# Kernel tuning notes

Measured on AMD Instinct MI355X. Metric: run time of the kernel, lower is better.

## Reference

```python
import jax, jax.numpy as jnp
import numpy as np


def setup_inputs() -> dict:
    key = jax.random.key(0)
    ks = jax.random.split(key, 16)
    B, T, H, E, V = 64, 512, 512, 512, 50257
    sc = 0.02  # weight init scale
    return {
        "enc_seq": jax.random.normal(ks[0], (B, T, H), jnp.float32),
        "enc_mask": jax.random.randint(ks[1], (B, T), 0, 2).astype(jnp.int32),
        "h0": jax.random.normal(ks[2], (1, B, H), jnp.float32),
        "c0": jax.random.normal(ks[3], (1, B, H), jnp.float32),
        "bos_id": 1,
        "eos_id": 2,
        "max_len": 28,
        "emb": jax.random.normal(ks[4], (V, E), jnp.float32) * sc,
        "W_h": jax.random.normal(ks[5], (H, H), jnp.float32) * sc,
        "W_s": jax.random.normal(ks[6], (H, H), jnp.float32) * sc,
        "v": jax.random.normal(ks[7], (H,), jnp.float32) * sc,
        "W_ih": jax.random.normal(ks[8], (4 * H, E + H), jnp.float32) * sc,
        "W_hh": jax.random.normal(ks[9], (4 * H, H), jnp.float32) * sc,
        "b_ih": jnp.zeros((4 * H,), jnp.float32),
        "b_hh": jnp.zeros((4 * H,), jnp.float32),
        "W_out": jax.random.normal(ks[10], (V, H), jnp.float32) * sc,
        "b_out": jnp.zeros((V,), jnp.float32),
    }


def reference(enc_seq, enc_mask, h0, c0, bos_id, eos_id, max_len,
              emb, W_h, W_s, v, W_ih, W_hh, b_ih, b_hh, W_out, b_out):
    B = enc_seq.shape[0]
    h = h0[0]  # [B, H]  (torch: transpose(0,1).squeeze(1))
    c = c0[0]
    # W_h(enc_seq) is loop-invariant; precompute once (same math as per-step recompute)
    Wh_enc = jnp.einsum('bth,kh->btk', enc_seq, W_h)  # [B, T, H]
    neg_inf = jnp.float32(-1e9)
    y0 = jnp.full((B,), bos_id, dtype=jnp.int32)

    def step(carry, _):
        h, c, y = carry
        e_t = emb[y]                                            # [B, E]
        s = h @ W_s.T                                           # [B, H]
        scores = jnp.einsum('bth,h->bt', jnp.tanh(Wh_enc + s[:, None, :]), v)
        scores = jnp.where(enc_mask == 0, neg_inf, scores)
        a = jax.nn.softmax(scores, axis=1)                      # [B, T]
        ctx = jnp.einsum('bt,bth->bh', a, enc_seq)              # [B, H]
        x = jnp.concatenate([e_t, ctx], axis=-1)                # [B, E+H]
        gates = x @ W_ih.T + h @ W_hh.T + b_ih + b_hh           # [B, 4H]
        i, f, g, o = jnp.split(gates, 4, axis=-1)               # torch gate order i,f,g,o
        c2 = jax.nn.sigmoid(f) * c + jax.nn.sigmoid(i) * jnp.tanh(g)
        h2 = jax.nn.sigmoid(o) * jnp.tanh(c2)
        # dropout is identity in eval mode (greedy decoding)
        logits = h2 @ W_out.T + b_out                           # [B, V]
        y2 = jnp.argmax(logits, axis=-1).astype(jnp.int32)
        return (h2, c2, y2), y2

    _, ys = jax.lax.scan(step, (h, c, y0), None, length=max_len - 1)
    return ys.T  # [B, max_len-1] greedy token ids
```

## Files before the change

kernel.cpp:

```cpp
#include <hip/hip_runtime.h>
#include <hip/hip_bf16.h>
#include <cmath>


#define TKK 16

__global__ __launch_bounds__(256) void gemm_tile(
    const float* __restrict__ A, int lda,
    const float* __restrict__ B, int ldb,
    float* __restrict__ C, int ldc,
    int Kchunk, long long c_zstride)
{
  __shared__ __align__(16) float At[TKK][68];
  __shared__ __align__(16) float Bt[TKK][132];
  const int tid = threadIdx.x;
  const int tx = tid & 15, ty = tid >> 4;
  const long long mbase = (long long)blockIdx.y * 64;
  const long long nbase = (long long)blockIdx.x * 128;
  const int kbase = blockIdx.z * Kchunk;
  const float* Ap = A + mbase * lda + kbase;
  const float* Bp = B + nbase * ldb + kbase;
  float acc[4][8];
#pragma unroll
  for (int i = 0; i < 4; i++)
#pragma unroll
    for (int j = 0; j < 8; j++) acc[i][j] = 0.f;

  const int lm = tid >> 2;
  const int lk = (tid & 3) << 2;
  for (int k0 = 0; k0 < Kchunk; k0 += TKK) {
    float4 av = *(const float4*)(Ap + (long long)lm * lda + k0 + lk);
    At[lk + 0][lm] = av.x; At[lk + 1][lm] = av.y;
    At[lk + 2][lm] = av.z; At[lk + 3][lm] = av.w;
#pragma unroll
    for (int r = 0; r < 2; r++) {
      int n = (tid + r * 256) >> 2;
      float4 bv = *(const float4*)(Bp + (long long)n * ldb + k0 + lk);
      Bt[lk + 0][n] = bv.x; Bt[lk + 1][n] = bv.y;
      Bt[lk + 2][n] = bv.z; Bt[lk + 3][n] = bv.w;
    }
    __syncthreads();
#pragma unroll
    for (int kk = 0; kk < TKK; ++kk) {
      float4 a4 = *(const float4*)&At[kk][ty * 4];
      float4 b0 = *(const float4*)&Bt[kk][tx * 8];
      float4 b1 = *(const float4*)&Bt[kk][tx * 8 + 4];
      float as[4] = {a4.x, a4.y, a4.z, a4.w};
      float bs[8] = {b0.x, b0.y, b0.z, b0.w, b1.x, b1.y, b1.z, b1.w};
#pragma unroll
      for (int i = 0; i < 4; i++)
#pragma unroll
        for (int j = 0; j < 8; j++)
          acc[i][j] = fmaf(as[i], bs[j], acc[i][j]);
    }
    __syncthreads();
  }
  float* Cp = C + (long long)blockIdx.z * c_zstride;
#pragma unroll
  for (int i = 0; i < 4; i++) {
    long long m = mbase + ty * 4 + i;
#pragma unroll
    for (int j = 0; j < 8; j += 4) {
      float4 v;
      v.x = acc[i][j]; v.y = acc[i][j + 1]; v.z = acc[i][j + 2]; v.w = acc[i][j + 3];
      *(float4*)(Cp + m * ldc + nbase + tx * 8 + j) = v;
    }
  }
}

__global__ __launch_bounds__(256) void wcat_kernel(
    const float* __restrict__ W_ih, const float* __restrict__ W_hh,
    float* __restrict__ wcat)
{
  long long fi = (long long)blockIdx.x * 256 + threadIdx.x;
  if (fi >= 2048LL * 1536 / 4) return;
  int k = (int)(fi / 384);
  int c = (int)(fi % 384) * 4;
  float4 v;
  if (c < 1024) v = *(const float4*)(W_ih + (long long)k * 1024 + c);
  else          v = *(const float4*)(W_hh + (long long)k * 512 + (c - 1024));
  *(float4*)(wcat + fi * 4) = v;
}

__global__ __launch_bounds__(256) void init_kernel(
    const float* __restrict__ h0, const float* __restrict__ c0,
    const int* __restrict__ bos,
    float* __restrict__ h, float* __restrict__ c, int* __restrict__ y)
{
  int i = blockIdx.x * 256 + threadIdx.x;
  if (i < 64 * 512) { h[i] = h0[i]; c[i] = c0[i]; }
  if (i < 64) y[i] = bos[0];
}

__global__ __launch_bounds__(256) void scores_kernel(
    const float* __restrict__ whenc,
    const float* __restrict__ spart,
    const float* __restrict__ vvec,
    const int* __restrict__ mask,
    float* __restrict__ scores)
{
  const int b = blockIdx.x, tc = blockIdx.y, tid = threadIdx.x;
  __shared__ __align__(16) float sS[512];
  __shared__ __align__(16) float sV[512];
  for (int i = tid; i < 512; i += 256) {
    sS[i] = spart[0 * 64 * 512 + b * 512 + i] + spart[1 * 64 * 512 + b * 512 + i]
          + spart[2 * 64 * 512 + b * 512 + i] + spart[3 * 64 * 512 + b * 512 + i];
    sV[i] = vvec[i];
  }
  __syncthreads();
  const int wave = tid >> 6, lane = tid & 63;
  const int t0 = tc * 128 + wave * 32;
  for (int tt = 0; tt < 32; ++tt) {
    int t = t0 + tt;
    const float* row = whenc + ((long long)b * 512 + t) * 512;
    float p = 0.f;
#pragma unroll
    for (int u = 0; u < 2; ++u) {
      int hb = u * 256 + lane * 4;
      float4 w = *(const float4*)(row + hb);
      float4 s4 = *(const float4*)&sS[hb];
      float4 v4 = *(const float4*)&sV[hb];
      p = fmaf(v4.x, tanhf(w.x + s4.x), p);
      p = fmaf(v4.y, tanhf(w.y + s4.y), p);
      p = fmaf(v4.z, tanhf(w.z + s4.z), p);
      p = fmaf(v4.w, tanhf(w.w + s4.w), p);
    }
#pragma unroll
    for (int off = 32; off; off >>= 1) p += __shfl_xor(p, off);
    if (lane == 0)
      scores[b * 512 + t] = mask[b * 512 + t] ? p : -1e9f;
  }
}

__global__ __launch_bounds__(256) void ctx_kernel(
    const float* __restrict__ scores,
    const float* __restrict__ enc,
    float* __restrict__ ctxp)
{
  const int b = blockIdx.x, tc = blockIdx.y, tid = threadIdx.x;
  __shared__ float sc[512];
  __shared__ float red[256];
  float l0 = scores[b * 512 + tid];
  float l1 = scores[b * 512 + 256 + tid];
  red[tid] = fmaxf(l0, l1);
  __syncthreads();
  for (int s = 128; s > 0; s >>= 1) {
    if (tid < s) red[tid] = fmaxf(red[tid], red[tid + s]);
    __syncthreads();
  }
  float mx = red[0];
  __syncthreads();
  float e0 = expf(l0 - mx), e1 = expf(l1 - mx);
  sc[tid] = e0; sc[tid + 256] = e1;
  red[tid] = e0 + e1;
  __syncthreads();
  for (int s = 128; s > 0; s >>= 1) {
    if (tid < s) red[tid] += red[tid + s];
    __syncthreads();
  }
  float inv = 1.f / red[0];
  float a0 = 0.f, a1 = 0.f;
  for (int u = 0; u < 128; ++u) {
    int t = tc * 128 + u;
    float w = sc[t] * inv;
    const float* row = enc + ((long long)b * 512 + t) * 512;
    float2 e = *(const float2*)(row + tid * 2);
    a0 = fmaf(w, e.x, a0);
    a1 = fmaf(w, e.y, a1);
  }
  float2 o; o.x = a0; o.y = a1;
  *(float2*)(ctxp + ((long long)(b * 4 + tc)) * 512 + tid * 2) = o;
}

__global__ __launch_bounds__(256) void xbuild_kernel(
    const float* __restrict__ emb, const int* __restrict__ y,
    const float* __restrict__ ctxp, const float* __restrict__ h,
    float* __restrict__ x)
{
  const int b = blockIdx.x, tid = threadIdx.x;
  const int yb = y[b];
  for (int i = tid; i < 1536; i += 256) {
    float val;
    if (i < 512) {
      val = emb[(long long)yb * 512 + i];
    } else if (i < 1024) {
      int hh = i - 512;
      val = ctxp[(b * 4 + 0) * 512 + hh] + ctxp[(b * 4 + 1) * 512 + hh]
          + ctxp[(b * 4 + 2) * 512 + hh] + ctxp[(b * 4 + 3) * 512 + hh];
    } else {
      val = h[b * 512 + (i - 1024)];
    }
    x[b * 1536 + i] = val;
  }
}

__global__ __launch_bounds__(512) void lstm_kernel(
    const float* __restrict__ gpart,
    const float* __restrict__ b_ih, const float* __restrict__ b_hh,
    float* __restrict__ h, float* __restrict__ c)
{
  const int b = blockIdx.x, hc = threadIdx.x;
  float g[4];
#pragma unroll
  for (int q = 0; q < 4; q++) {
    int k = q * 512 + hc;
    float s = b_ih[k] + b_hh[k];
    s += gpart[(0 * 64 + b) * 2048 + k];
    s += gpart[(1 * 64 + b) * 2048 + k];
    s += gpart[(2 * 64 + b) * 2048 + k];
    g[q] = s;
  }
  float ig = 1.f / (1.f + expf(-g[0]));
  float fg = 1.f / (1.f + expf(-g[1]));
  float gg = tanhf(g[2]);
  float og = 1.f / (1.f + expf(-g[3]));
  float c2 = fg * c[b * 512 + hc] + ig * gg;
  float h2 = og * tanhf(c2);
  c[b * 512 + hc] = c2;
  h[b * 512 + hc] = h2;
}

__global__ __launch_bounds__(256) void logits_kernel(
    const float* __restrict__ A,
    const float* __restrict__ W,
    const float* __restrict__ bias,
    int V, float* __restrict__ pval, int* __restrict__ pidx, int nvc)
{
  __shared__ __align__(16) float At[TKK][68];
  __shared__ __align__(16) float Bt[TKK][132];
  __shared__ float lv[64][16];
  __shared__ int   li[64][16];
  const int tid = threadIdx.x;
  const int tx = tid & 15, ty = tid >> 4;
  const int nbase = blockIdx.x * 128;
  float acc[4][8];
#pragma unroll
  for (int i = 0; i < 4; i++)
#pragma unroll
    for (int j = 0; j < 8; j++) acc[i][j] = 0.f;
  const int lm = tid >> 2;
  const int lk = (tid & 3) << 2;
  for (int k0 = 0; k0 < 512; k0 += TKK) {
    float4 av = *(const float4*)(A + lm * 512 + k0 + lk);
    At[lk + 0][lm] = av.x; At[lk + 1][lm] = av.y;
    At[lk + 2][lm] = av.z; At[lk + 3][lm] = av.w;
#pragma unroll
    for (int r = 0; r < 2; r++) {
      int n = (tid + r * 256) >> 2;
      int ng = nbase + n;
      float4 bv = make_float4(0.f, 0.f, 0.f, 0.f);
      if (ng < V) bv = *(const float4*)(W + (long long)ng * 512 + k0 + lk);
      Bt[lk + 0][n] = bv.x; Bt[lk + 1][n] = bv.y;
      Bt[lk + 2][n] = bv.z; Bt[lk + 3][n] = bv.w;
    }
    __syncthreads();
#pragma unroll
    for (int kk = 0; kk < TKK; ++kk) {
      float4 a4 = *(const float4*)&At[kk][ty * 4];
      float4 b0 = *(const float4*)&Bt[kk][tx * 8];
      float4 b1 = *(const float4*)&Bt[kk][tx * 8 + 4];
      float as[4] = {a4.x, a4.y, a4.z, a4.w};
      float bs[8] = {b0.x, b0.y, b0.z, b0.w, b1.x, b1.y, b1.z, b1.w};
#pragma unroll
      for (int i = 0; i < 4; i++)
#pragma unroll
        for (int j = 0; j < 8; j++)
          acc[i][j] = fmaf(as[i], bs[j], acc[i][j]);
    }
    __syncthreads();
  }
#pragma unroll
  for (int i = 0; i < 4; i++) {
    float bv_ = -INFINITY; int bi_ = 0x7fffffff;
#pragma unroll
    for (int j = 0; j < 8; j++) {
      int vg = nbase + tx * 8 + j;
      if (vg < V) {
        float val = acc[i][j] + bias[vg];
        if (val > bv_) { bv_ = val; bi_ = vg; }
      }
    }
    lv[ty * 4 + i][tx] = bv_; li[ty * 4 + i][tx] = bi_;
  }
  __syncthreads();
  if (tid < 64) {
    float bv_ = -INFINITY; int bi_ = 0x7fffffff;
#pragma unroll
    for (int t = 0; t < 16; t++) {
      if (lv[tid][t] > bv_) { bv_ = lv[tid][t]; bi_ = li[tid][t]; }
    }
    pval[tid * nvc + blockIdx.x] = bv_;
    pidx[tid * nvc + blockIdx.x] = bi_;
  }
}

__global__ __launch_bounds__(64) void argfinal_kernel(
    const float* __restrict__ pval, const int* __restrict__ pidx, int nvc,
    int* __restrict__ y, int* __restrict__ out, int step, int steps)
{
  const int b = blockIdx.x, lane = threadIdx.x;
  float bv = -INFINITY; int bi = 0x7fffffff;
  for (int ci = lane; ci < nvc; ci += 64) {
    float v = pval[b * nvc + ci];
    int ix = pidx[b * nvc + ci];
    if (v > bv || (v == bv && ix < bi)) { bv = v; bi = ix; }
  }
#pragma unroll
  for (int off = 32; off; off >>= 1) {
    float ov = __shfl_xor(bv, off);
    int oi = __shfl_xor(bi, off);
    if (ov > bv || (ov == bv && oi < bi)) { bv = ov; bi = oi; }
  }
  if (lane == 0) { y[b] = bi; out[b * steps + step] = bi; }
}

extern "C" void kernel_launch(void* const* d_in, const int* in_sizes, int n_in,
                              void* d_out, int out_size, void* d_ws, size_t ws_size,
                              hipStream_t stream) {
  const float* enc_seq = (const float*)d_in[0];
  const int*   enc_mask = (const int*)d_in[1];
  const float* h0 = (const float*)d_in[2];
  const float* c0 = (const float*)d_in[3];
  const int*   bos = (const int*)d_in[4];
  const float* emb = (const float*)d_in[7];
  const float* W_h = (const float*)d_in[8];
  const float* W_s = (const float*)d_in[9];
  const float* vvec = (const float*)d_in[10];
  const float* W_ih = (const float*)d_in[11];
  const float* W_hh = (const float*)d_in[12];
  const float* b_ih = (const float*)d_in[13];
  const float* b_hh = (const float*)d_in[14];
  const float* W_out = (const float*)d_in[15];
  const float* b_out = (const float*)d_in[16];

  const int B = 64, T = 512, H = 512;
  const int V = in_sizes[16];
  const int steps = out_size / B;
  const int NVC = (V + 127) / 128;
  int* out = (int*)d_out;

  float* ws = (float*)d_ws;
  size_t off = 0;
  auto alloc = [&](size_t n) { float* p = ws + off; off += (n + 15) & ~(size_t)15; return p; };
  float* whenc  = alloc((size_t)B * T * H);
  float* scores = alloc((size_t)B * T);
  float* spart  = alloc(4ull * B * H);
  float* ctxp   = alloc((size_t)B * 4 * H);
  float* xbuf   = alloc((size_t)B * 1536);
  float* gpart  = alloc(3ull * B * 2048);
  float* wcat   = alloc(2048ull * 1536);
  float* hbuf   = alloc((size_t)B * H);
  float* cbuf   = alloc((size_t)B * H);
  float* pval   = alloc((size_t)B * NVC);
  int*   ybuf   = (int*)alloc(B);
  int*   pidx   = (int*)alloc((size_t)B * NVC);
  (void)ws_size;

  init_kernel<<<128, 256, 0, stream>>>(h0, c0, bos, hbuf, cbuf, ybuf);
  wcat_kernel<<<3072, 256, 0, stream>>>(W_ih, W_hh, wcat);

  gemm_tile<<<dim3(4, 512, 1), 256, 0, stream>>>(
      enc_seq, 512, W_h, 512, whenc, 512, 512, 0);

  for (int step = 0; step < steps; ++step) {
    gemm_tile<<<dim3(4, 1, 4), 256, 0, stream>>>(
        hbuf, 512, W_s, 512, spart, 512, 128, (long long)B * H);
    scores_kernel<<<dim3(64, 4), 256, 0, stream>>>(whenc, spart, vvec, enc_mask, scores);
    ctx_kernel<<<dim3(64, 4), 256, 0, stream>>>(scores, enc_seq, ctxp);
    xbuild_kernel<<<64, 256, 0, stream>>>(emb, ybuf, ctxp, hbuf, xbuf);
    gemm_tile<<<dim3(16, 1, 3), 256, 0, stream>>>(
        xbuf, 1536, wcat, 1536, gpart, 2048, 512, (long long)B * 2048);
    lstm_kernel<<<64, 512, 0, stream>>>(gpart, b_ih, b_hh, hbuf, cbuf);
    logits_kernel<<<NVC, 256, 0, stream>>>(hbuf, W_out, b_out, V, pval, pidx, NVC);
    argfinal_kernel<<<64, 64, 0, stream>>>(pval, pidx, NVC, ybuf, out, step, steps);
  }
}
```

Before: 6.069 ms.

## Use split-bf16 MFMA for per-step GEMMs and logits with fused argmax

```diff
diff --git a/kernel.cpp b/kernel.cpp
--- a/kernel.cpp
+++ b/kernel.cpp
@@ -4,6 +4,20 @@
 
 
 #define TKK 16
+
+typedef __attribute__((ext_vector_type(8))) short bf16x8;
+typedef __attribute__((ext_vector_type(4))) float f32x4;
+
+__device__ inline unsigned short bf16rn(float x) {
+  unsigned int u = __float_as_uint(x);
+  unsigned int r = u + 0x7fffu + ((u >> 16) & 1u);
+  return (unsigned short)(r >> 16);
+}
+__device__ inline void split1(float x, unsigned short& h, unsigned short& l) {
+  h = bf16rn(x);
+  float hf = __uint_as_float(((unsigned int)h) << 16);
+  l = bf16rn(x - hf);
+}
 
 __global__ __launch_bounds__(256) void gemm_tile(
     const float* __restrict__ A, int lda,
@@ -43,8 +57,8 @@
 #pragma unroll
     for (int kk = 0; kk < TKK; ++kk) {
       float4 a4 = *(const float4*)&At[kk][ty * 4];
-      float4 b0 = *(const float4*)&Bt[kk][tx * 8];
-      float4 b1 = *(const float4*)&Bt[kk][tx * 8 + 4];
+      float4 b0 = *(const float4*)&Bt[kk][tx * 4];
+      float4 b1 = *(const float4*)&Bt[kk][64 + tx * 4];
       float as[4] = {a4.x, a4.y, a4.z, a4.w};
       float bs[8] = {b0.x, b0.y, b0.z, b0.w, b1.x, b1.y, b1.z, b1.w};
 #pragma unroll
@@ -59,12 +73,11 @@
 #pragma unroll
   for (int i = 0; i < 4; i++) {
     long long m = mbase + ty * 4 + i;
-#pragma unroll
-    for (int j = 0; j < 8; j += 4) {
-      float4 v;
-      v.x = acc[i][j]; v.y = acc[i][j + 1]; v.z = acc[i][j + 2]; v.w = acc[i][j + 3];
-      *(float4*)(Cp + m * ldc + nbase + tx * 8 + j) = v;
-    }
+    float4 v0, v1;
+    v0.x = acc[i][0]; v0.y = acc[i][1]; v0.z = acc[i][2]; v0.w = acc[i][3];
+    v1.x = acc[i][4]; v1.y = acc[i][5]; v1.z = acc[i][6]; v1.w = acc[i][7];
+    *(float4*)(Cp + m * ldc + nbase + tx * 4) = v0;
+    *(float4*)(Cp + m * ldc + nbase + 64 + tx * 4) = v1;
   }
 }
 
@@ -82,19 +95,62 @@
   *(float4*)(wcat + fi * 4) = v;
 }
 
+__global__ __launch_bounds__(256) void wcat_split_kernel(
+    const float* __restrict__ W_ih, const float* __restrict__ W_hh,
+    unsigned short* __restrict__ whi, unsigned short* __restrict__ wlo)
+{
+  long long fi = (long long)blockIdx.x * 256 + threadIdx.x;
+  if (fi >= 2048LL * 1536 / 4) return;
+  int k = (int)(fi / 384);
+  int c = (int)(fi % 384) * 4;
+  float4 v;
+  if (c < 1024) v = *(const float4*)(W_ih + (long long)k * 1024 + c);
+  else          v = *(const float4*)(W_hh + (long long)k * 512 + (c - 1024));
+  long long e = fi * 4;
+  float xs[4] = {v.x, v.y, v.z, v.w};
+#pragma unroll
+  for (int q = 0; q < 4; q++) {
+    unsigned short h, l; split1(xs[q], h, l);
+    whi[e + q] = h; wlo[e + q] = l;
+  }
+}
+
+__global__ __launch_bounds__(256) void split_kernel(
+    const float* __restrict__ src, unsigned short* __restrict__ hi,
+    unsigned short* __restrict__ lo, long long n)
+{
+  long long i = (long long)blockIdx.x * 256 + threadIdx.x;
+  long long stride = (long long)gridDim.x * 256;
+  for (long long e = i * 4; e < n; e += stride * 4) {
+    float4 v = *(const float4*)(src + e);
+    float xs[4] = {v.x, v.y, v.z, v.w};
+#pragma unroll
+    for (int q = 0; q < 4; q++) {
+      unsigned short h, l; split1(xs[q], h, l);
+      hi[e + q] = h; lo[e + q] = l;
+    }
+  }
+}
+
 __global__ __launch_bounds__(256) void init_kernel(
     const float* __restrict__ h0, const float* __restrict__ c0,
     const int* __restrict__ bos,
-    float* __restrict__ h, float* __restrict__ c, int* __restrict__ y)
+    float* __restrict__ h, float* __restrict__ c, int* __restrict__ y,
+    unsigned short* __restrict__ h_hi, unsigned short* __restrict__ h_lo)
 {
   int i = blockIdx.x * 256 + threadIdx.x;
-  if (i < 64 * 512) { h[i] = h0[i]; c[i] = c0[i]; }
+  if (i < 64 * 512) {
+    float hv = h0[i];
+    h[i] = hv; c[i] = c0[i];
+    unsigned short hh, hl; split1(hv, hh, hl);
+    h_hi[i] = hh; h_lo[i] = hl;
+  }
   if (i < 64) y[i] = bos[0];
 }
 
 __global__ __launch_bounds__(256) void scores_kernel(
     const float* __restrict__ whenc,
-    const float* __restrict__ spart,
+    const float* __restrict__ spart, int np,
     const float* __restrict__ vvec,
     const int* __restrict__ mask,
     float* __restrict__ scores)
@@ -103,8 +159,9 @@
   __shared__ __align__(16) float sS[512];
   __shared__ __align__(16) float sV[512];
   for (int i = tid; i < 512; i += 256) {
-    sS[i] = spart[0 * 64 * 512 + b * 512 + i] + spart[1 * 64 * 512 + b * 512 + i]
-          + spart[2 * 64 * 512 + b * 512 + i] + spart[3 * 64 * 512 + b * 512 + i];
+    float s = 0.f;
+    for (int p = 0; p < np; ++p) s += spart[(long long)p * 64 * 512 + b * 512 + i];
+    sS[i] = s;
     sV[i] = vvec[i];
   }
   __syncthreads();
@@ -175,7 +232,8 @@
 __global__ __launch_bounds__(256) void xbuild_kernel(
     const float* __restrict__ emb, const int* __restrict__ y,
     const float* __restrict__ ctxp, const float* __restrict__ h,
-    float* __restrict__ x)
+    float* __restrict__ xf,
+    unsigned short* __restrict__ xhi, unsigned short* __restrict__ xlo)
 {
   const int b = blockIdx.x, tid = threadIdx.x;
   const int yb = y[b];
@@ -190,14 +248,19 @@
     } else {
       val = h[b * 512 + (i - 1024)];
     }
-    x[b * 1536 + i] = val;
+    if (xf) xf[b * 1536 + i] = val;
+    if (xhi) {
+      unsigned short hh2, ll2; split1(val, hh2, ll2);
+      xhi[b * 1536 + i] = hh2; xlo[b * 1536 + i] = ll2;
+    }
   }
 }
 
 __global__ __launch_bounds__(512) void lstm_kernel(
-    const float* __restrict__ gpart,
+    const float* __restrict__ gpart, int ngparts,
     const float* __restrict__ b_ih, const float* __restrict__ b_hh,
-    float* __restrict__ h, float* __restrict__ c)
+    float* __restrict__ h, float* __restrict__ c,
+    unsigned short* __restrict__ h_hi, unsigned short* __restrict__ h_lo)
 {
   const int b = blockIdx.x, hc = threadIdx.x;
   float g[4];
@@ -205,9 +268,8 @@
   for (int q = 0; q < 4; q++) {
     int k = q * 512 + hc;
     float s = b_ih[k] + b_hh[k];
-    s += gpart[(0 * 64 + b) * 2048 + k];
-    s += gpart[(1 * 64 + b) * 2048 + k];
-    s += gpart[(2 * 64 + b) * 2048 + k];
+    for (int p = 0; p < ngparts; ++p)
+      s += gpart[((long long)p * 64 + b) * 2048 + k];
     g[q] = s;
   }
   float ig = 1.f / (1.f + expf(-g[0]));
@@ -218,6 +280,105 @@
   float h2 = og * tanhf(c2);
   c[b * 512 + hc] = c2;
   h[b * 512 + hc] = h2;
+  if (h_hi) {
+    unsigned short hh, hl; split1(h2, hh, hl);
+    h_hi[b * 512 + hc] = hh; h_lo[b * 512 + hc] = hl;
+  }
+}
+
+__global__ __launch_bounds__(256) void mfma_gemm(
+    const unsigned short* __restrict__ Ahi, const unsigned short* __restrict__ Alo,
+    const unsigned short* __restrict__ Bhi, const unsigned short* __restrict__ Blo,
+    float* __restrict__ C, int K, int N)
+{
+  const int tid = threadIdx.x;
+  const int w = tid >> 6, l = tid & 63;
+  const int arow = blockIdx.y * 64 + w * 16 + (l & 15);
+  const int koff = (l >> 4) * 8;
+  const int nbase = blockIdx.x * 64;
+  f32x4 acc[4];
+#pragma unroll
+  for (int cf = 0; cf < 4; ++cf) acc[cf] = (f32x4){0.f, 0.f, 0.f, 0.f};
+
+  for (int k0 = 0; k0 < K; k0 += 32) {
+    bf16x8 ahi = *(const bf16x8*)(Ahi + (size_t)arow * K + k0 + koff);
+    bf16x8 alo = *(const bf16x8*)(Alo + (size_t)arow * K + k0 + koff);
+#pragma unroll
+    for (int cf = 0; cf < 4; ++cf) {
+      int col = nbase + cf * 16 + (l & 15);
+      bf16x8 bhi = *(const bf16x8*)(Bhi + (size_t)col * K + k0 + koff);
+      bf16x8 blo = *(const bf16x8*)(Blo + (size_t)col * K + k0 + koff);
+      acc[cf] = __builtin_amdgcn_mfma_f32_16x16x32_bf16(ahi, bhi, acc[cf], 0, 0, 0);
+      acc[cf] = __builtin_amdgcn_mfma_f32_16x16x32_bf16(ahi, blo, acc[cf], 0, 0, 0);
+      acc[cf] = __builtin_amdgcn_mfma_f32_16x16x32_bf16(alo, bhi, acc[cf], 0, 0, 0);
+    }
+  }
+#pragma unroll
+  for (int cf = 0; cf < 4; ++cf) {
+    int col = nbase + cf * 16 + (l & 15);
+#pragma unroll
+    for (int j = 0; j < 4; ++j) {
+      int rowc = blockIdx.y * 64 + w * 16 + (l >> 4) * 4 + j;
+      C[(size_t)rowc * N + col] = acc[cf][j];
+    }
+  }
+}
+
+__global__ __launch_bounds__(256) void mfma_logits(
+    const unsigned short* __restrict__ Ahi, const unsigned short* __restrict__ Alo,
+    const unsigned short* __restrict__ Bhi, const unsigned short* __restrict__ Blo,
+    const float* __restrict__ bias, int V, int K,
+    float* __restrict__ pval, int* __restrict__ pidx, int nvc)
+{
+  const int tid = threadIdx.x;
+  const int w = tid >> 6, l = tid & 63;
+  const int arow = w * 16 + (l & 15);
+  const int koff = (l >> 4) * 8;
+  const int nbase = blockIdx.x * 64;
+  const bf16x8 bz = {0, 0, 0, 0, 0, 0, 0, 0};
+  f32x4 acc[4];
+#pragma unroll
+  for (int cf = 0; cf < 4; ++cf) acc[cf] = (f32x4){0.f, 0.f, 0.f, 0.f};
+
+  for (int k0 = 0; k0 < K; k0 += 32) {
+    bf16x8 ahi = *(const bf16x8*)(Ahi + (size_t)arow * K + k0 + koff);
+    bf16x8 alo = *(const bf16x8*)(Alo + (size_t)arow * K + k0 + koff);
+#pragma unroll
+    for (int cf = 0; cf < 4; ++cf) {
+      int col = nbase + cf * 16 + (l & 15);
+      bf16x8 bhi = bz, blo = bz;
+      if (col < V) {
+        bhi = *(const bf16x8*)(Bhi + (size_t)col * K + k0 + koff);
+        blo = *(const bf16x8*)(Blo + (size_t)col * K + k0 + koff);
+      }
+      acc[cf] = __builtin_amdgcn_mfma_f32_16x16x32_bf16(ahi, bhi, acc[cf], 0, 0, 0);
+      acc[cf] = __builtin_amdgcn_mfma_f32_16x16x32_bf16(ahi, blo, acc[cf], 0, 0, 0);
+      acc[cf] = __builtin_amdgcn_mfma_f32_16x16x32_bf16(alo, bhi, acc[cf], 0, 0, 0);
+    }
+  }
+#pragma unroll
+  for (int j = 0; j < 4; ++j) {
+    float bv = -INFINITY; int bi = 0x7fffffff;
+#pragma unroll
+    for (int cf = 0; cf < 4; ++cf) {
+      int col = nbase + cf * 16 + (l & 15);
+      if (col < V) {
+        float v = acc[cf][j] + bias[col];
+        if (v > bv) { bv = v; bi = col; }
+      }
+    }
+#pragma unroll
+    for (int off = 1; off <= 8; off <<= 1) {
+      float ov = __shfl_xor(bv, off);
+      int oi = __shfl_xor(bi, off);
+      if (ov > bv || (ov == bv && oi < bi)) { bv = ov; bi = oi; }
+    }
+    if ((l & 15) == 0) {
+      int b = w * 16 + (l >> 4) * 4 + j;
+      pval[b * nvc + blockIdx.x] = bv;
+      pidx[b * nvc + blockIdx.x] = bi;
+    }
+  }
 }
 
 __global__ __launch_bounds__(256) void logits_kernel(
@@ -257,8 +418,8 @@
 #pragma unroll
     for (int kk = 0; kk < TKK; ++kk) {
       float4 a4 = *(const float4*)&At[kk][ty * 4];
-      float4 b0 = *(const float4*)&Bt[kk][tx * 8];
-      float4 b1 = *(const float4*)&Bt[kk][tx * 8 + 4];
+      float4 b0 = *(const float4*)&Bt[kk][tx * 4];
+      float4 b1 = *(const float4*)&Bt[kk][64 + tx * 4];
       float as[4] = {a4.x, a4.y, a4.z, a4.w};
       float bs[8] = {b0.x, b0.y, b0.z, b0.w, b1.x, b1.y, b1.z, b1.w};
 #pragma unroll
@@ -274,10 +435,10 @@
     float bv_ = -INFINITY; int bi_ = 0x7fffffff;
 #pragma unroll
     for (int j = 0; j < 8; j++) {
-      int vg = nbase + tx * 8 + j;
+      int vg = (j < 4) ? (nbase + tx * 4 + j) : (nbase + 64 + tx * 4 + (j - 4));
       if (vg < V) {
         float val = acc[i][j] + bias[vg];
-        if (val > bv_) { bv_ = val; bi_ = vg; }
+        if (val > bv_ || (val == bv_ && vg < bi_)) { bv_ = val; bi_ = vg; }
       }
     }
     lv[ty * 4 + i][tx] = bv_; li[ty * 4 + i][tx] = bi_;
@@ -287,7 +448,9 @@
     float bv_ = -INFINITY; int bi_ = 0x7fffffff;
 #pragma unroll
     for (int t = 0; t < 16; t++) {
-      if (lv[tid][t] > bv_) { bv_ = lv[tid][t]; bi_ = li[tid][t]; }
+      if (lv[tid][t] > bv_ || (lv[tid][t] == bv_ && li[tid][t] < bi_)) {
+        bv_ = lv[tid][t]; bi_ = li[tid][t];
+      }
     }
     pval[tid * nvc + blockIdx.x] = bv_;
     pidx[tid * nvc + blockIdx.x] = bi_;
@@ -334,44 +497,101 @@
   const float* b_out = (const float*)d_in[16];
 
   const int B = 64, T = 512, H = 512;
-  const int V = in_sizes[16];
+  const int Vn = in_sizes[15] / 512;
   const int steps = out_size / B;
-  const int NVC = (V + 127) / 128;
   int* out = (int*)d_out;
 
   float* ws = (float*)d_ws;
   size_t off = 0;
   auto alloc = [&](size_t n) { float* p = ws + off; off += (n + 15) & ~(size_t)15; return p; };
-  float* whenc  = alloc((size_t)B * T * H);
-  float* scores = alloc((size_t)B * T);
-  float* spart  = alloc(4ull * B * H);
-  float* ctxp   = alloc((size_t)B * 4 * H);
-  float* xbuf   = alloc((size_t)B * 1536);
-  float* gpart  = alloc(3ull * B * 2048);
-  float* wcat   = alloc(2048ull * 1536);
-  float* hbuf   = alloc((size_t)B * H);
-  float* cbuf   = alloc((size_t)B * H);
-  float* pval   = alloc((size_t)B * NVC);
-  int*   ybuf   = (int*)alloc(B);
-  int*   pidx   = (int*)alloc((size_t)B * NVC);
-  (void)ws_size;
-
-  init_kernel<<<128, 256, 0, stream>>>(h0, c0, bos, hbuf, cbuf, ybuf);
-  wcat_kernel<<<3072, 256, 0, stream>>>(W_ih, W_hh, wcat);
-
-  gemm_tile<<<dim3(4, 512, 1), 256, 0, stream>>>(
-      enc_seq, 512, W_h, 512, whenc, 512, 512, 0);
-
-  for (int step = 0; step < steps; ++step) {
-    gemm_tile<<<dim3(4, 1, 4), 256, 0, stream>>>(
-        hbuf, 512, W_s, 512, spart, 512, 128, (long long)B * H);
-    scores_kernel<<<dim3(64, 4), 256, 0, stream>>>(whenc, spart, vvec, enc_mask, scores);
-    ctx_kernel<<<dim3(64, 4), 256, 0, stream>>>(scores, enc_seq, ctxp);
-    xbuild_kernel<<<64, 256, 0, stream>>>(emb, ybuf, ctxp, hbuf, xbuf);
-    gemm_tile<<<dim3(16, 1, 3), 256, 0, stream>>>(
-        xbuf, 1536, wcat, 1536, gpart, 2048, 512, (long long)B * 2048);
-    lstm_kernel<<<64, 512, 0, stream>>>(gpart, b_ih, b_hh, hbuf, cbuf);
-    logits_kernel<<<NVC, 256, 0, stream>>>(hbuf, W_out, b_out, V, pval, pidx, NVC);
-    argfinal_kernel<<<64, 64, 0, stream>>>(pval, pidx, NVC, ybuf, out, step, steps);
-  }
-}
+
+  const size_t NEW_NEED = 200ull << 20;
+  if (ws_size >= NEW_NEED) {
+    const int NVC = (Vn + 63) / 64;
+    float* whenc  = alloc((size_t)B * T * H);
+    float* sbuf   = alloc((size_t)B * T);
+    float* spartf = alloc((size_t)B * H);
+    float* ctxp   = alloc((size_t)B * 4 * H);
+    float* gbuf   = alloc((size_t)B * 2048);
+    float* hbuf   = alloc((size_t)B * H);
+    float* cbuf   = alloc((size_t)B * H);
+    float* pval   = alloc((size_t)B * NVC);
+    int*   pidx   = (int*)alloc((size_t)B * NVC);
+    int*   ybuf   = (int*)alloc(B);
+    unsigned short* h_hi  = (unsigned short*)alloc((size_t)B * H / 2);
+    unsigned short* h_lo  = (unsigned short*)alloc((size_t)B * H / 2);
+    unsigned short* x_hi  = (unsigned short*)alloc((size_t)B * 1536 / 2);
+    unsigned short* x_lo  = (unsigned short*)alloc((size_t)B * 1536 / 2);
+    unsigned short* ws_hi = (unsigned short*)alloc(512ull * 512 / 2);
+    unsigned short* ws_lo = (unsigned short*)alloc(512ull * 512 / 2);
+    unsigned short* wc_hi = (unsigned short*)alloc(2048ull * 1536 / 2);
+    unsigned short* wc_lo = (unsigned short*)alloc(2048ull * 1536 / 2);
+    unsigned short* wo_hi = (unsigned short*)alloc((size_t)Vn * 512 / 2);
+    unsigned short* wo_lo = (unsigned short*)alloc((size_t)Vn * 512 / 2);
+
+    init_kernel<<<128, 256, 0, stream>>>(h0, c0, bos, hbuf, cbuf, ybuf, h_hi, h_lo);
+    wcat_split_kernel<<<3072, 256, 0, stream>>>(W_ih, W_hh, wc_hi, wc_lo);
+    split_kernel<<<256, 256, 0, stream>>>(W_s, ws_hi, ws_lo, 512ll * 512);
+    split_kernel<<<4096, 256, 0, stream>>>(W_out, wo_hi, wo_lo, (long long)Vn * 512);
+
+    gemm_tile<<<dim3(4, 512, 1), 256, 0, stream>>>(
+        enc_seq, 512, W_h, 512, whenc, 512, 512, 0);
+
+    for (int step = 0; step < steps; ++step) {
+      mfma_gemm<<<dim3(8, 1), 256, 0, stream>>>(h_hi, h_lo, ws_hi, ws_lo,
+                                                spartf, 512, 512);
+      scores_kernel<<<dim3(64, 4), 256, 0, stream>>>(whenc, spartf, 1, vvec,
+                                                     enc_mask, sbuf);
+      ctx_kernel<<<dim3(64, 4), 256, 0, stream>>>(sbuf, enc_seq, ctxp);
+      xbuild_kernel<<<64, 256, 0, stream>>>(emb, ybuf, ctxp, hbuf,
+                                            nullptr, x_hi, x_lo);
+      mfma_gemm<<<dim3(32, 1), 256, 0, stream>>>(x_hi, x_lo, wc_hi, wc_lo,
+                                                 gbuf, 1536, 2048);
+      lstm_kernel<<<64, 512, 0, stream>>>(gbuf, 1, b_ih, b_hh, hbuf, cbuf,
+                                          h_hi, h_lo);
+      mfma_logits<<<NVC, 256, 0, stream>>>(h_hi, h_lo, wo_hi, wo_lo, b_out,
+                                           Vn, 512, pval, pidx, NVC);
+      argfinal_kernel<<<64, 64, 0, stream>>>(pval, pidx, NVC, ybuf, out,
+                                             step, steps);
+    }
+  } else {
+    const int NVC = (Vn + 127) / 128;
+    float* whenc  = alloc((size_t)B * T * H);
+    float* sbuf   = alloc((size_t)B * T);
+    float* spart  = alloc(4ull * B * H);
+    float* ctxp   = alloc((size_t)B * 4 * H);
+    float* xbuf   = alloc((size_t)B * 1536);
+    float* gpart  = alloc(3ull * B * 2048);
+    float* wcat   = alloc(2048ull * 1536);
+    float* hbuf   = alloc((size_t)B * H);
+    float* cbuf   = alloc((size_t)B * H);
+    float* pval   = alloc((size_t)B * NVC);
+    int*   ybuf   = (int*)alloc(B);
+    int*   pidx   = (int*)alloc((size_t)B * NVC);
+    unsigned short* h_hi = (unsigned short*)alloc((size_t)B * H / 2);
+    unsigned short* h_lo = (unsigned short*)alloc((size_t)B * H / 2);
+
+    init_kernel<<<128, 256, 0, stream>>>(h0, c0, bos, hbuf, cbuf, ybuf, h_hi, h_lo);
+    wcat_kernel<<<3072, 256, 0, stream>>>(W_ih, W_hh, wcat);
+    gemm_tile<<<dim3(4, 512, 1), 256, 0, stream>>>(
+        enc_seq, 512, W_h, 512, whenc, 512, 512, 0);
+
+    for (int step = 0; step < steps; ++step) {
+      gemm_tile<<<dim3(4, 1, 4), 256, 0, stream>>>(
+          hbuf, 512, W_s, 512, spart, 512, 128, (long long)B * H);
+      scores_kernel<<<dim3(64, 4), 256, 0, stream>>>(whenc, spart, 4, vvec,
+                                                     enc_mask, sbuf);
+      ctx_kernel<<<dim3(64, 4), 256, 0, stream>>>(sbuf, enc_seq, ctxp);
+      xbuild_kernel<<<64, 256, 0, stream>>>(emb, ybuf, ctxp, hbuf,
+                                            xbuf, nullptr, nullptr);
+      gemm_tile<<<dim3(16, 1, 3), 256, 0, stream>>>(
+          xbuf, 1536, wcat, 1536, gpart, 2048, 512, (long long)B * 2048);
+      lstm_kernel<<<64, 512, 0, stream>>>(gpart, 3, b_ih, b_hh, hbuf, cbuf,
+                                          nullptr, nullptr);
+      logits_kernel<<<NVC, 256, 0, stream>>>(hbuf, W_out, b_out, Vn,
+                                             pval, pidx, NVC);
+      argfinal_kernel<<<64, 64, 0, stream>>>(pval, pidx, NVC, ybuf, out,
+                                             step, steps);
+    }
+  }
+}
```

Result: slower. 6.973 ms (+14.9%).
